# Optimization experiments

Measured on AMD Instinct MI355X. Metric: run time of the kernel, lower is better.

Reference implementation:

```python
import math
import jax, jax.numpy as jnp
import numpy as np
from jax import lax

B, T, D, H = 4, 1024, 1024, 8192
EPS = 1e-6
PLIF_TH = 0.05        # plif_threshold init
SURR_ALPHA = 2.0      # atan surrogate sharpness
SPARSITY = 0.95

@jax.custom_vjp
def spike(v):
    # Heaviside forward, atan surrogate backward (spikingjelly-style)
    return (v > 0).astype(v.dtype)

def _spike_fwd(v):
    return (v > 0).astype(v.dtype), v

def _spike_bwd(v, g):
    return (g * (SURR_ALPHA / 2.0) / (1.0 + (math.pi / 2.0 * SURR_ALPHA * v) ** 2),)

spike.defvjp(_spike_fwd, _spike_bwd)

def rmsnorm(x, w):
    return x * lax.rsqrt(jnp.mean(x * x, axis=-1, keepdims=True) + EPS) * w

def setup_inputs() -> dict:
    key = jax.random.key(0)
    ks = jax.random.split(key, 12)
    std = 0.02
    return {
        "x": jax.random.normal(ks[0], (B, T, D), jnp.float32),
        "ln1_w": jnp.ones((D,), jnp.float32),
        "liq_Wi": jax.random.normal(ks[1], (D, D), jnp.float32) * std,
        "liq_Wr": jax.random.normal(ks[2], (D, D), jnp.float32) * std,
        "liq_b": jnp.zeros((D,), jnp.float32),
        "liq_tau": 0.5 + jax.random.uniform(ks[3], (D,), jnp.float32),  # positive time constants ('hasani' init)
        "plif_tau": jnp.full((1,), 2.5, jnp.float32),                   # plif_tau_init=2.5
        "syn_w": jax.random.normal(ks[4], (D, D), jnp.float32) * std,
        "gate_w": jax.random.normal(ks[5], (D, D), jnp.float32) * 0.01,
        "gate_b": jnp.zeros((D,), jnp.float32),
        "ln2_w": jnp.ones((D,), jnp.float32),
        "ffn_wg": jax.random.normal(ks[6], (H, D), jnp.float32) * std,
        "ffn_wu": jax.random.normal(ks[7], (H, D), jnp.float32) * std,
        "ffn_wd": jax.random.normal(ks[8], (D, H), jnp.float32) * (std / math.sqrt(2.0)),
        "syn_mask": jax.random.uniform(ks[9], (D, D), jnp.float32) < (1.0 - SPARSITY),
    }

def _forward(x, ln1_w, liq_Wi, liq_Wr, liq_b, liq_tau, plif_tau,
             syn_w, gate_w, gate_b, ln2_w, ffn_wg, ffn_wu, ffn_wd, syn_mask):
    a = rmsnorm(x, ln1_w)                                   # (B,T,D)
    # LiquidCell: ODE-style leaky recurrence, h_t = h*e^{-1/tau} + (1-e^{-1/tau})*tanh(Wi x + Wr h + b)
    decay = jnp.exp(-1.0 / liq_tau)                         # (D,)
    def liq_step(h, xt):
        f = jnp.tanh(xt @ liq_Wi.T + h @ liq_Wr.T + liq_b)
        h2 = h * decay + (1.0 - decay) * f
        return h2, h2
    _, hs = lax.scan(liq_step, jnp.zeros((B, D), x.dtype), jnp.swapaxes(a, 0, 1))
    h = jnp.swapaxes(hs, 0, 1)                              # (B,T,D)
    # PLIFCell.forward_seq: v += (h_t - v)/tau; spike; subtract reset
    inv_tau = 1.0 / plif_tau[0]
    def plif_step(v, ht):
        v = v + (ht - v) * inv_tau
        s = spike(v - PLIF_TH)
        return v - s * PLIF_TH, s
    _, ss = lax.scan(plif_step, jnp.zeros((B, D), x.dtype), jnp.swapaxes(h, 0, 1))
    s = jnp.swapaxes(ss, 0, 1)                              # (B,T,D) binary spikes
    w_eff = syn_w * syn_mask.astype(syn_w.dtype)
    syn_out = s @ w_eff.T
    gated = syn_out * jax.nn.sigmoid(s @ gate_w.T + gate_b)
    x = x + gated
    y = rmsnorm(x, ln2_w)
    ffn = (jax.nn.silu(y @ ffn_wg.T) * (y @ ffn_wu.T)) @ ffn_wd.T
    return x + ffn

def reference(x, ln1_w, liq_Wi, liq_Wr, liq_b, liq_tau, plif_tau,
              syn_w, gate_w, gate_b, ln2_w, ffn_wg, ffn_wu, ffn_wd, syn_mask):
    return _forward(x, ln1_w, liq_Wi, liq_Wr, liq_b, liq_tau, plif_tau,
                    syn_w, gate_w, gate_b, ln2_w, ffn_wg, ffn_wu, ffn_wd, syn_mask)
```

## Files before the change

kernel.cpp:

```cpp
#include <hip/hip_runtime.h>
#include <math.h>


#define Bsz 4
#define Tsz 1024
#define Dsz 1024
#define Hsz 8192

typedef __attribute__((ext_vector_type(8))) short short8;
typedef __attribute__((ext_vector_type(4))) float floatx4_t;


__device__ __forceinline__ unsigned short f2bf(float f) {
  union { float f; unsigned u; } c; c.f = f;
  unsigned x = c.u;
  unsigned r = (x + 0x7FFFu + ((x >> 16) & 1u)) >> 16;
  return (unsigned short)r;
}

__device__ __forceinline__ void gll16(const void* gsrc, void* ldst) {
  __builtin_amdgcn_global_load_lds(
      (const __attribute__((address_space(1))) unsigned int*)gsrc,
      (__attribute__((address_space(3))) unsigned int*)ldst,
      16, 0, 0);
}


__global__ void zero_u64_k(unsigned long long* p, int n) {
  int i = blockIdx.x * 256 + threadIdx.x;
  if (i < n) p[i] = 0ull;
}

__global__ void detect_mask_k(const unsigned int* m, int* mode) {
  if (blockIdx.x == 0 && threadIdx.x == 0) {
    int md = 0;
    for (int i = 0; i < 256; ++i) {
      unsigned w = m[i];
      if (w == 0x3F800000u) { md = 2; break; }
      if (w > 1u) md = 1;
    }
    *mode = md;
  }
}

__global__ void cvt_bf16_k(const float* __restrict__ in,
                           unsigned short* __restrict__ out, int n4) {
  int i = blockIdx.x * 256 + threadIdx.x;
  if (i < n4) {
    float4 v = ((const float4*)in)[i];
    ushort4 o;
    o.x = f2bf(v.x); o.y = f2bf(v.y); o.z = f2bf(v.z); o.w = f2bf(v.w);
    ((ushort4*)out)[i] = o;
  }
}

__global__ void make_weff_k(const float* __restrict__ syn,
                            const void* __restrict__ mask,
                            const int* __restrict__ mode,
                            unsigned short* __restrict__ out, int n) {
  int i = blockIdx.x * 256 + threadIdx.x;
  if (i < n) {
    int md = *mode;
    bool on;
    if (md == 1)      on = ((const unsigned char*)mask)[i] != 0;
    else if (md == 2) on = ((const float*)mask)[i] != 0.f;
    else              on = ((const int*)mask)[i] != 0;
    out[i] = on ? f2bf(syn[i]) : (unsigned short)0;
  }
}


template<int BF16OUT>
__global__ __launch_bounds__(256)
void rmsnorm_k(const float* __restrict__ X, const float* __restrict__ w,
               void* __restrict__ out) {
  const long row = blockIdx.x;
  const float* x = X + row * Dsz;
  float4 v = ((const float4*)x)[threadIdx.x];
  float ss = v.x * v.x + v.y * v.y + v.z * v.z + v.w * v.w;
#pragma unroll
  for (int off = 32; off > 0; off >>= 1) ss += __shfl_down(ss, off);
  __shared__ float red[4];
  if ((threadIdx.x & 63) == 0) red[threadIdx.x >> 6] = ss;
  __syncthreads();
  float tot = red[0] + red[1] + red[2] + red[3];
  float scale = 1.0f / sqrtf(tot * (1.0f / Dsz) + 1e-6f);
  float4 wv = ((const float4*)w)[threadIdx.x];
  float o0 = v.x * scale * wv.x, o1 = v.y * scale * wv.y;
  float o2 = v.z * scale * wv.z, o3 = v.w * scale * wv.w;
  if (BF16OUT) {
    ushort4 o; o.x = f2bf(o0); o.y = f2bf(o1); o.z = f2bf(o2); o.w = f2bf(o3);
    ((ushort4*)out)[row * 256 + threadIdx.x] = o;
  } else {
    float4 o; o.x = o0; o.y = o1; o.z = o2; o.w = o3;
    ((float4*)out)[row * 256 + threadIdx.x] = o;
  }
}


__global__ __launch_bounds__(256)
void gemm_f32_bt(const float* __restrict__ A, const float* __restrict__ Bm,
                 const float* __restrict__ bias, float* __restrict__ C,
                 int M, int N, int K) {
  __shared__ float sA[16][128 + 4];
  __shared__ float sB[16][64 + 4];
  const int bm = blockIdx.x, bn = blockIdx.y;
  const int tid = threadIdx.x;
  const int tx = tid & 15, ty = tid >> 4;
  float cacc[8][4] = {};
  for (int k0 = 0; k0 < K; k0 += 16) {
#pragma unroll
    for (int i = 0; i < 2; ++i) {
      int slot = tid * 2 + i, row = slot >> 2, kq = slot & 3;
      float4 v = *(const float4*)(A + (long)(bm * 128 + row) * K + k0 + kq * 4);
      sA[kq * 4 + 0][row] = v.x; sA[kq * 4 + 1][row] = v.y;
      sA[kq * 4 + 2][row] = v.z; sA[kq * 4 + 3][row] = v.w;
    }
    {
      int row = tid >> 2, kq = tid & 3;
      float4 v = *(const float4*)(Bm + (long)(bn * 64 + row) * K + k0 + kq * 4);
      sB[kq * 4 + 0][row] = v.x; sB[kq * 4 + 1][row] = v.y;
      sB[kq * 4 + 2][row] = v.z; sB[kq * 4 + 3][row] = v.w;
    }
    __syncthreads();
#pragma unroll
    for (int kk = 0; kk < 16; ++kk) {
      float4 A0 = *(const float4*)&sA[kk][ty * 8];
      float4 A1 = *(const float4*)&sA[kk][ty * 8 + 4];
      float4 B0 = *(const float4*)&sB[kk][tx * 4];
      float av[8] = {A0.x, A0.y, A0.z, A0.w, A1.x, A1.y, A1.z, A1.w};
      float bv[4] = {B0.x, B0.y, B0.z, B0.w};
#pragma unroll
      for (int r = 0; r < 8; ++r)
#pragma unroll
        for (int c = 0; c < 4; ++c) cacc[r][c] += av[r] * bv[c];
    }
    __syncthreads();
  }
#pragma unroll
  for (int r = 0; r < 8; ++r) {
#pragma unroll
    for (int c = 0; c < 4; ++c) {
      int col = bn * 64 + tx * 4 + c;
      C[(long)(bm * 128 + ty * 8 + r) * N + col] = cacc[r][c] + bias[col];
    }
  }
}


__global__ __launch_bounds__(256)
void liquid_plif_k(const float* __restrict__ Wr, const float* __restrict__ U,
                   const float* __restrict__ liq_tau,
                   const float* __restrict__ plif_tau,
                   unsigned long long* __restrict__ Hex,
                   unsigned short* __restrict__ Sout) {
  const int blk = blockIdx.x;
  const int b = blk >> 5;
  const int base = (blk & 31) * 32;
  const int tid = threadIdx.x;
  const int rg = tid & 7;
  const int ck = tid >> 3;

  __shared__ float h_lds[1024];
  __shared__ float red[4][8][4];

  float4 wr[4][8];
#pragma unroll
  for (int r = 0; r < 4; ++r) {
    const float* wrow = Wr + (long)(base + rg * 4 + r) * Dsz + ck * 32;
#pragma unroll
    for (int qq = 0; qq < 8; ++qq) {
      int q = (qq + ck) & 7;
      wr[r][qq] = *(const float4*)(wrow + q * 4);
    }
  }

  float hstate = 0.f, vstate = 0.f, dec = 0.f, omdec = 0.f, itau = 0.f;
  if (tid < 32) {
    float tau = liq_tau[base + tid];
    dec = expf(-1.0f / tau);
    omdec = 1.0f - dec;
    itau = 1.0f / plif_tau[0];
  }

  for (int t = 1; t <= Tsz; ++t) {
    float uval = 0.f;
    if (tid < 32)
      uval = U[((long)b * Tsz + (t - 1)) * Dsz + base + tid];

    const unsigned want = (unsigned)(t - 1);
    const unsigned long long* src = Hex + (((long)((t - 1) & 1) * Bsz + b) << 10);
    unsigned long long a0, a1, a2, a3;
    for (;;) {
      a0 = __hip_atomic_load(src + tid,       __ATOMIC_RELAXED, __HIP_MEMORY_SCOPE_AGENT);
      a1 = __hip_atomic_load(src + tid + 256, __ATOMIC_RELAXED, __HIP_MEMORY_SCOPE_AGENT);
      a2 = __hip_atomic_load(src + tid + 512, __ATOMIC_RELAXED, __HIP_MEMORY_SCOPE_AGENT);
      a3 = __hip_atomic_load(src + tid + 768, __ATOMIC_RELAXED, __HIP_MEMORY_SCOPE_AGENT);
      if ((unsigned)(a0 >> 32) == want && (unsigned)(a1 >> 32) == want &&
          (unsigned)(a2 >> 32) == want && (unsigned)(a3 >> 32) == want)
        break;
      __builtin_amdgcn_s_sleep(1);
    }
    h_lds[tid]       = __uint_as_float((unsigned)a0);
    h_lds[tid + 256] = __uint_as_float((unsigned)a1);
    h_lds[tid + 512] = __uint_as_float((unsigned)a2);
    h_lds[tid + 768] = __uint_as_float((unsigned)a3);
    __syncthreads();

    float acc0 = 0.f, acc1 = 0.f, acc2 = 0.f, acc3 = 0.f;
    const float* hch = &h_lds[ck * 32];
#pragma unroll
    for (int qq = 0; qq < 8; ++qq) {
      const int q = (qq + ck) & 7;
      float4 hv = *(const float4*)(hch + q * 4);
      acc0 += wr[0][qq].x * hv.x + wr[0][qq].y * hv.y + wr[0][qq].z * hv.z + wr[0][qq].w * hv.w;
      acc1 += wr[1][qq].x * hv.x + wr[1][qq].y * hv.y + wr[1][qq].z * hv.z + wr[1][qq].w * hv.w;
      acc2 += wr[2][qq].x * hv.x + wr[2][qq].y * hv.y + wr[2][qq].z * hv.z + wr[2][qq].w * hv.w;
      acc3 += wr[3][qq].x * hv.x + wr[3][qq].y * hv.y + wr[3][qq].z * hv.z + wr[3][qq].w * hv.w;
    }
    acc0 += __shfl_xor(acc0, 8);  acc0 += __shfl_xor(acc0, 16); acc0 += __shfl_xor(acc0, 32);
    acc1 += __shfl_xor(acc1, 8);  acc1 += __shfl_xor(acc1, 16); acc1 += __shfl_xor(acc1, 32);
    acc2 += __shfl_xor(acc2, 8);  acc2 += __shfl_xor(acc2, 16); acc2 += __shfl_xor(acc2, 32);
    acc3 += __shfl_xor(acc3, 8);  acc3 += __shfl_xor(acc3, 16); acc3 += __shfl_xor(acc3, 32);
    if ((tid & 56) == 0) {
      const int wv = tid >> 6;
      red[wv][rg][0] = acc0; red[wv][rg][1] = acc1;
      red[wv][rg][2] = acc2; red[wv][rg][3] = acc3;
    }
    __syncthreads();

    if (tid < 32) {
      const int r2 = tid >> 2, jj = tid & 3;
      float sum = red[0][r2][jj] + red[1][r2][jj] + red[2][r2][jj] + red[3][r2][jj];
      float f = tanhf(sum + uval);
      hstate = hstate * dec + omdec * f;
      vstate += (hstate - vstate) * itau;
      float sp = ((vstate - 0.05f) > 0.f) ? 1.f : 0.f;
      vstate -= sp * 0.05f;
      unsigned long long pv =
          (((unsigned long long)(unsigned)t) << 32) |
          (unsigned long long)__float_as_uint(hstate);
      __hip_atomic_store(&Hex[(((long)(t & 1) * Bsz + b) << 10) + base + tid], pv,
                         __ATOMIC_RELAXED, __HIP_MEMORY_SCOPE_AGENT);
      Sout[((long)b * Tsz + (t - 1)) * Dsz + base + tid] =
          (sp > 0.f) ? (unsigned short)0x3F80 : (unsigned short)0;
    }
  }
}


template<int NB, int EPI>
__global__ __launch_bounds__(256)
void gemm_bt(const unsigned short* __restrict__ A,
             const unsigned short* __restrict__ B0,
             const unsigned short* __restrict__ B1,
             const float* __restrict__ aux0, const float* __restrict__ aux1,
             void* __restrict__ outp, int M, int N, int K) {
  __shared__ unsigned short sA[128 * 32];
  __shared__ unsigned short sB[2 * 128 * 32];
  const int tid = threadIdx.x;
  const int w = tid >> 6, l = tid & 63;
  const int wm = w & 1, wn = w >> 1;
  const int bm = blockIdx.x, bn = blockIdx.y;

  floatx4_t acc[NB][4][4];
#pragma unroll
  for (int j = 0; j < NB; ++j)
#pragma unroll
    for (int m = 0; m < 4; ++m)
#pragma unroll
      for (int n = 0; n < 4; ++n) acc[j][m][n] = (floatx4_t)(0.f);

  const int rA = bm * 128 + 16 * w + (l >> 2);
  const int rB = bn * 128 + 16 * w + (l >> 2);
  const int kl = (l & 3) * 8;
  const unsigned short* gA = A + (long)rA * K + kl;
  const unsigned short* gB0 = B0 + (long)rB * K + kl;
  const unsigned short* gB1 = nullptr;
  if constexpr (NB > 1) gB1 = B1 + (long)rB * K + kl;
  unsigned short* lA = &sA[(16 * w) * 32];
  unsigned short* lB = &sB[(16 * w) * 32];

  for (int k0 = 0; k0 < K; k0 += 32) {
    gll16(gA + k0,              lA);
    gll16(gA + k0 + 64 * K,     lA + 64 * 32);
    gll16(gB0 + k0,             lB);
    gll16(gB0 + k0 + 64 * K,    lB + 64 * 32);
    if constexpr (NB > 1) {
      gll16(gB1 + k0,           lB + 128 * 32);
      gll16(gB1 + k0 + 64 * K,  lB + 192 * 32);
    }
    __syncthreads();
    short8 af[4];
#pragma unroll
    for (int m = 0; m < 4; ++m)
      af[m] = *(const short8*)&sA[(wm * 64 + m * 16 + (l & 15)) * 32 + (l >> 4) * 8];
#pragma unroll
    for (int j = 0; j < NB; ++j) {
#pragma unroll
      for (int n = 0; n < 4; ++n) {
        short8 bf = *(const short8*)&sB[j * 128 * 32 +
                        (wn * 64 + n * 16 + (l & 15)) * 32 + (l >> 4) * 8];
#pragma unroll
        for (int m = 0; m < 4; ++m)
          acc[j][m][n] = __builtin_amdgcn_mfma_f32_16x16x32_bf16(
              af[m], bf, acc[j][m][n], 0, 0, 0);
      }
    }
    __syncthreads();
  }

  const int colBase = bn * 128 + wn * 64;
  const int rowBase = bm * 128 + wm * 64;
#pragma unroll
  for (int m = 0; m < 4; ++m) {
#pragma unroll
    for (int n = 0; n < 4; ++n) {
      const int col = colBase + n * 16 + (l & 15);
#pragma unroll
      for (int j = 0; j < 4; ++j) {
        const int row = rowBase + m * 16 + (l >> 4) * 4 + j;
        const long idx = (long)row * N + col;
        float v0 = acc[0][m][n][j];
        if constexpr (EPI == 1) {
          float gsum = acc[NB - 1][m][n][j] + aux1[col];
          float sg = 1.f / (1.f + __expf(-gsum));
          ((float*)outp)[idx] = aux0[idx] + v0 * sg;
        } else if constexpr (EPI == 2) {
          float sil = v0 / (1.f + __expf(-v0));
          ((unsigned short*)outp)[idx] = f2bf(sil * acc[NB - 1][m][n][j]);
        } else {
          ((float*)outp)[idx] = aux0[idx] + v0;
        }
      }
    }
  }
}


extern "C" void kernel_launch(void* const* d_in, const int* in_sizes, int n_in,
                              void* d_out, int out_size, void* d_ws, size_t ws_size,
                              hipStream_t stream) {
  (void)in_sizes; (void)n_in; (void)out_size; (void)ws_size;

  const float* x        = (const float*)d_in[0];
  const float* ln1_w    = (const float*)d_in[1];
  const float* liq_Wi   = (const float*)d_in[2];
  const float* liq_Wr   = (const float*)d_in[3];
  const float* liq_b    = (const float*)d_in[4];
  const float* liq_tau  = (const float*)d_in[5];
  const float* plif_tau = (const float*)d_in[6];
  const float* syn_w    = (const float*)d_in[7];
  const float* gate_w   = (const float*)d_in[8];
  const float* gate_b   = (const float*)d_in[9];
  const float* ln2_w    = (const float*)d_in[10];
  const float* ffn_wg   = (const float*)d_in[11];
  const float* ffn_wu   = (const float*)d_in[12];
  const float* ffn_wd   = (const float*)d_in[13];
  const void*  mask     = d_in[14];

  char* ws = (char*)d_ws;
  const size_t MB = 1024ull * 1024ull;
  unsigned short* wg_bf   = (unsigned short*)(ws + 0 * MB);
  unsigned short* wu_bf   = (unsigned short*)(ws + 16 * MB);
  unsigned short* wd_bf   = (unsigned short*)(ws + 32 * MB);
  unsigned short* weff_bf = (unsigned short*)(ws + 48 * MB);
  unsigned short* gw_bf   = (unsigned short*)(ws + 50 * MB);
  float*          x2_f    = (float*)         (ws + 52 * MB);
  unsigned short* s_bf    = (unsigned short*)(ws + 68 * MB);
  unsigned short* y_bf    = (unsigned short*)(ws + 76 * MB);
  unsigned short* ff_bf   = (unsigned short*)(ws + 84 * MB);
  float*          a_f     = (float*)         (ws + 84 * MB);
  float*          u_f     = (float*)         (ws + 100 * MB);
  unsigned long long* hex = (unsigned long long*)(ws + 148 * MB);
  int*            mode    = (int*)(ws + 148 * MB + 65536);
  float*          out_f   = (float*)d_out;

  const int M = Bsz * Tsz;

  detect_mask_k<<<1, 64, 0, stream>>>((const unsigned int*)mask, mode);
  cvt_bf16_k<<<(Hsz * Dsz / 4) / 256, 256, 0, stream>>>(ffn_wg, wg_bf, Hsz * Dsz / 4);
  cvt_bf16_k<<<(Hsz * Dsz / 4) / 256, 256, 0, stream>>>(ffn_wu, wu_bf, Hsz * Dsz / 4);
  cvt_bf16_k<<<(Dsz * Hsz / 4) / 256, 256, 0, stream>>>(ffn_wd, wd_bf, Dsz * Hsz / 4);
  cvt_bf16_k<<<(Dsz * Dsz / 4) / 256, 256, 0, stream>>>(gate_w, gw_bf, Dsz * Dsz / 4);
  make_weff_k<<<(Dsz * Dsz) / 256, 256, 0, stream>>>(syn_w, mask, mode, weff_bf, Dsz * Dsz);
  zero_u64_k<<<32, 256, 0, stream>>>(hex, 2 * Bsz * Dsz);

  rmsnorm_k<0><<<M, 256, 0, stream>>>(x, ln1_w, a_f);

  gemm_f32_bt<<<dim3(M / 128, Dsz / 64), 256, 0, stream>>>(
      a_f, liq_Wi, liq_b, u_f, M, Dsz, Dsz);

  liquid_plif_k<<<128, 256, 0, stream>>>(liq_Wr, u_f, liq_tau, plif_tau, hex, s_bf);

  gemm_bt<2, 1><<<dim3(M / 128, Dsz / 128), 256, 0, stream>>>(
      s_bf, weff_bf, gw_bf, x, gate_b, x2_f, M, Dsz, Dsz);

  rmsnorm_k<1><<<M, 256, 0, stream>>>(x2_f, ln2_w, y_bf);

  gemm_bt<2, 2><<<dim3(M / 128, Hsz / 128), 256, 0, stream>>>(
      y_bf, wg_bf, wu_bf, nullptr, nullptr, ff_bf, M, Hsz, Dsz);

  gemm_bt<1, 3><<<dim3(M / 128, Dsz / 128), 256, 0, stream>>>(
      ff_bf, wd_bf, nullptr, x2_f, nullptr, out_f, M, Dsz, Hsz);
}
```

Measured before the change: 2.449 ms.

## Co-locate recurrence blocks per batch on one XCD and poll with L2-local loads

The grid is doubled to 256 and odd-XCD blocks exit, so that all 32 blocks serving one batch index sit on a single XCD, assuming round-robin block-to-XCD placement. The spin-wait first polls with volatile loads that may hit the shared L2, and falls back to agent-scope atomic loads after two rounds. Each producer writes with a volatile store followed by the atomic store. tanhf is replaced by a fast exp/rcp formula. The goal is lower cross-XCD synchronization latency per timestep, at the risk of relying on undocumented block placement and on volatile-visibility semantics, and of a small precision loss in tanh.

```diff
diff --git a/kernel.cpp b/kernel.cpp
--- a/kernel.cpp
+++ b/kernel.cpp
@@ -155,8 +155,10 @@
                    unsigned long long* __restrict__ Hex,
                    unsigned short* __restrict__ Sout) {
   const int blk = blockIdx.x;
-  const int b = blk >> 5;
-  const int base = (blk & 31) * 32;
+  const int xcd = blk & 7;
+  if (xcd & 1) return;
+  const int b = xcd >> 1;
+  const int base = (blk >> 3) * 32;
   const int tid = threadIdx.x;
   const int rg = tid & 7;
   const int ck = tid >> 3;
@@ -190,16 +192,27 @@
 
     const unsigned want = (unsigned)(t - 1);
     const unsigned long long* src = Hex + (((long)((t - 1) & 1) * Bsz + b) << 10);
-    unsigned long long a0, a1, a2, a3;
-    for (;;) {
-      a0 = __hip_atomic_load(src + tid,       __ATOMIC_RELAXED, __HIP_MEMORY_SCOPE_AGENT);
-      a1 = __hip_atomic_load(src + tid + 256, __ATOMIC_RELAXED, __HIP_MEMORY_SCOPE_AGENT);
-      a2 = __hip_atomic_load(src + tid + 512, __ATOMIC_RELAXED, __HIP_MEMORY_SCOPE_AGENT);
-      a3 = __hip_atomic_load(src + tid + 768, __ATOMIC_RELAXED, __HIP_MEMORY_SCOPE_AGENT);
-      if ((unsigned)(a0 >> 32) == want && (unsigned)(a1 >> 32) == want &&
-          (unsigned)(a2 >> 32) == want && (unsigned)(a3 >> 32) == want)
-        break;
-      __builtin_amdgcn_s_sleep(1);
+    volatile const unsigned long long* vsrc = src;
+    unsigned long long a0 = 0, a1 = 0, a2 = 0, a3 = 0;
+    bool k0 = false, k1 = false, k2 = false, k3 = false;
+    for (int round = 0;; ++round) {
+      unsigned long long v;
+      if (!k0) { v = vsrc[tid      ]; if ((unsigned)(v >> 32) == want) { a0 = v; k0 = true; } }
+      if (!k1) { v = vsrc[tid + 256]; if ((unsigned)(v >> 32) == want) { a1 = v; k1 = true; } }
+      if (!k2) { v = vsrc[tid + 512]; if ((unsigned)(v >> 32) == want) { a2 = v; k2 = true; } }
+      if (!k3) { v = vsrc[tid + 768]; if ((unsigned)(v >> 32) == want) { a3 = v; k3 = true; } }
+      if (k0 && k1 && k2 && k3) break;
+      if (round >= 2) {
+        if (!k0) { v = __hip_atomic_load(src + tid,       __ATOMIC_RELAXED, __HIP_MEMORY_SCOPE_AGENT);
+                   if ((unsigned)(v >> 32) == want) { a0 = v; k0 = true; } }
+        if (!k1) { v = __hip_atomic_load(src + tid + 256, __ATOMIC_RELAXED, __HIP_MEMORY_SCOPE_AGENT);
+                   if ((unsigned)(v >> 32) == want) { a1 = v; k1 = true; } }
+        if (!k2) { v = __hip_atomic_load(src + tid + 512, __ATOMIC_RELAXED, __HIP_MEMORY_SCOPE_AGENT);
+                   if ((unsigned)(v >> 32) == want) { a2 = v; k2 = true; } }
+        if (!k3) { v = __hip_atomic_load(src + tid + 768, __ATOMIC_RELAXED, __HIP_MEMORY_SCOPE_AGENT);
+                   if ((unsigned)(v >> 32) == want) { a3 = v; k3 = true; } }
+        if (k0 && k1 && k2 && k3) break;
+      }
     }
     h_lds[tid]       = __uint_as_float((unsigned)a0);
     h_lds[tid + 256] = __uint_as_float((unsigned)a1);
@@ -232,15 +245,19 @@
     if (tid < 32) {
       const int r2 = tid >> 2, jj = tid & 3;
       float sum = red[0][r2][jj] + red[1][r2][jj] + red[2][r2][jj] + red[3][r2][jj];
-      float f = tanhf(sum + uval);
+      float z = sum + uval;
+      float ex = __expf(2.0f * z);
+      float f = 1.0f - 2.0f * __builtin_amdgcn_rcpf(ex + 1.0f);
       hstate = hstate * dec + omdec * f;
       vstate += (hstate - vstate) * itau;
       float sp = ((vstate - 0.05f) > 0.f) ? 1.f : 0.f;
       vstate -= sp * 0.05f;
+      const long pidx = (((long)(t & 1) * Bsz + b) << 10) + base + tid;
       unsigned long long pv =
           (((unsigned long long)(unsigned)t) << 32) |
           (unsigned long long)__float_as_uint(hstate);
-      __hip_atomic_store(&Hex[(((long)(t & 1) * Bsz + b) << 10) + base + tid], pv,
+      *(volatile unsigned long long*)&Hex[pidx] = pv;
+      __hip_atomic_store(&Hex[pidx], pv,
                          __ATOMIC_RELAXED, __HIP_MEMORY_SCOPE_AGENT);
       Sout[((long)b * Tsz + (t - 1)) * Dsz + base + tid] =
           (sp > 0.f) ? (unsigned short)0x3F80 : (unsigned short)0;
@@ -391,7 +408,7 @@
   gemm_f32_bt<<<dim3(M / 128, Dsz / 64), 256, 0, stream>>>(
       a_f, liq_Wi, liq_b, u_f, M, Dsz, Dsz);
 
-  liquid_plif_k<<<128, 256, 0, stream>>>(liq_Wr, u_f, liq_tau, plif_tau, hex, s_bf);
+  liquid_plif_k<<<256, 256, 0, stream>>>(liq_Wr, u_f, liq_tau, plif_tau, hex, s_bf);
 
   gemm_bt<2, 1><<<dim3(M / 128, Dsz / 128), 256, 0, stream>>>(
       s_bf, weff_bf, gw_bf, x, gate_b, x2_f, M, Dsz, Dsz);
```

Result: slower. 3.125 ms (+27.6%).

## Split liquid recurrence into producer waves and consumer wave with LDS flags

Applied to the files above, without the earlier changes.

Restructures the serial liquid/PLIF recurrence kernel. Four waves each poll only their own 256-element slice of the global h exchange buffer and compute partial matvecs. A dedicated fifth wave waits on workgroup-scope LDS flags, then does the tanh and state update. Block-wide __syncthreads barriers on each timestep are replaced by double-buffered reduction slots and release/acquire flags, and tanhf is swapped for a fast exp/rcp form. The aim is to shorten the per-step critical path, at the cost of spin-waiting and slightly lower tanh precision.

```diff
diff --git a/kernel.cpp b/kernel.cpp
--- a/kernel.cpp
+++ b/kernel.cpp
@@ -148,7 +148,7 @@
 }
 
 
-__global__ __launch_bounds__(256)
+__global__ __launch_bounds__(320)
 void liquid_plif_k(const float* __restrict__ Wr, const float* __restrict__ U,
                    const float* __restrict__ liq_tau,
                    const float* __restrict__ plif_tau,
@@ -158,92 +158,115 @@
   const int b = blk >> 5;
   const int base = (blk & 31) * 32;
   const int tid = threadIdx.x;
-  const int rg = tid & 7;
-  const int ck = tid >> 3;
 
   __shared__ float h_lds[1024];
-  __shared__ float red[4][8][4];
-
-  float4 wr[4][8];
-#pragma unroll
-  for (int r = 0; r < 4; ++r) {
-    const float* wrow = Wr + (long)(base + rg * 4 + r) * Dsz + ck * 32;
-#pragma unroll
-    for (int qq = 0; qq < 8; ++qq) {
-      int q = (qq + ck) & 7;
-      wr[r][qq] = *(const float4*)(wrow + q * 4);
-    }
-  }
-
-  float hstate = 0.f, vstate = 0.f, dec = 0.f, omdec = 0.f, itau = 0.f;
-  if (tid < 32) {
-    float tau = liq_tau[base + tid];
-    dec = expf(-1.0f / tau);
-    omdec = 1.0f - dec;
-    itau = 1.0f / plif_tau[0];
-  }
-
-  for (int t = 1; t <= Tsz; ++t) {
-    float uval = 0.f;
-    if (tid < 32)
-      uval = U[((long)b * Tsz + (t - 1)) * Dsz + base + tid];
-
-    const unsigned want = (unsigned)(t - 1);
-    const unsigned long long* src = Hex + (((long)((t - 1) & 1) * Bsz + b) << 10);
-    unsigned long long a0, a1, a2, a3;
-    for (;;) {
-      a0 = __hip_atomic_load(src + tid,       __ATOMIC_RELAXED, __HIP_MEMORY_SCOPE_AGENT);
-      a1 = __hip_atomic_load(src + tid + 256, __ATOMIC_RELAXED, __HIP_MEMORY_SCOPE_AGENT);
-      a2 = __hip_atomic_load(src + tid + 512, __ATOMIC_RELAXED, __HIP_MEMORY_SCOPE_AGENT);
-      a3 = __hip_atomic_load(src + tid + 768, __ATOMIC_RELAXED, __HIP_MEMORY_SCOPE_AGENT);
-      if ((unsigned)(a0 >> 32) == want && (unsigned)(a1 >> 32) == want &&
-          (unsigned)(a2 >> 32) == want && (unsigned)(a3 >> 32) == want)
-        break;
-      __builtin_amdgcn_s_sleep(1);
-    }
-    h_lds[tid]       = __uint_as_float((unsigned)a0);
-    h_lds[tid + 256] = __uint_as_float((unsigned)a1);
-    h_lds[tid + 512] = __uint_as_float((unsigned)a2);
-    h_lds[tid + 768] = __uint_as_float((unsigned)a3);
-    __syncthreads();
-
-    float acc0 = 0.f, acc1 = 0.f, acc2 = 0.f, acc3 = 0.f;
-    const float* hch = &h_lds[ck * 32];
-#pragma unroll
-    for (int qq = 0; qq < 8; ++qq) {
-      const int q = (qq + ck) & 7;
-      float4 hv = *(const float4*)(hch + q * 4);
-      acc0 += wr[0][qq].x * hv.x + wr[0][qq].y * hv.y + wr[0][qq].z * hv.z + wr[0][qq].w * hv.w;
-      acc1 += wr[1][qq].x * hv.x + wr[1][qq].y * hv.y + wr[1][qq].z * hv.z + wr[1][qq].w * hv.w;
-      acc2 += wr[2][qq].x * hv.x + wr[2][qq].y * hv.y + wr[2][qq].z * hv.z + wr[2][qq].w * hv.w;
-      acc3 += wr[3][qq].x * hv.x + wr[3][qq].y * hv.y + wr[3][qq].z * hv.z + wr[3][qq].w * hv.w;
-    }
-    acc0 += __shfl_xor(acc0, 8);  acc0 += __shfl_xor(acc0, 16); acc0 += __shfl_xor(acc0, 32);
-    acc1 += __shfl_xor(acc1, 8);  acc1 += __shfl_xor(acc1, 16); acc1 += __shfl_xor(acc1, 32);
-    acc2 += __shfl_xor(acc2, 8);  acc2 += __shfl_xor(acc2, 16); acc2 += __shfl_xor(acc2, 32);
-    acc3 += __shfl_xor(acc3, 8);  acc3 += __shfl_xor(acc3, 16); acc3 += __shfl_xor(acc3, 32);
-    if ((tid & 56) == 0) {
-      const int wv = tid >> 6;
-      red[wv][rg][0] = acc0; red[wv][rg][1] = acc1;
-      red[wv][rg][2] = acc2; red[wv][rg][3] = acc3;
-    }
-    __syncthreads();
-
-    if (tid < 32) {
-      const int r2 = tid >> 2, jj = tid & 3;
-      float sum = red[0][r2][jj] + red[1][r2][jj] + red[2][r2][jj] + red[3][r2][jj];
-      float f = tanhf(sum + uval);
-      hstate = hstate * dec + omdec * f;
-      vstate += (hstate - vstate) * itau;
-      float sp = ((vstate - 0.05f) > 0.f) ? 1.f : 0.f;
-      vstate -= sp * 0.05f;
-      unsigned long long pv =
-          (((unsigned long long)(unsigned)t) << 32) |
-          (unsigned long long)__float_as_uint(hstate);
-      __hip_atomic_store(&Hex[(((long)(t & 1) * Bsz + b) << 10) + base + tid], pv,
-                         __ATOMIC_RELAXED, __HIP_MEMORY_SCOPE_AGENT);
-      Sout[((long)b * Tsz + (t - 1)) * Dsz + base + tid] =
-          (sp > 0.f) ? (unsigned short)0x3F80 : (unsigned short)0;
+  __shared__ __align__(16) float red[2][4][8][4];
+  __shared__ int flags[2][4];
+
+  if (tid < 8) ((int*)flags)[tid] = 0;
+  __syncthreads();
+
+  if (tid < 256) {
+    const int l = tid & 63, w = tid >> 6;
+    const int rg = tid & 7;
+    const int ck = tid >> 3;
+    const int win = 256 * w;
+
+    float4 wr[4][8];
+#pragma unroll
+    for (int r = 0; r < 4; ++r) {
+      const float* wrow = Wr + (long)(base + rg * 4 + r) * Dsz + ck * 32;
+#pragma unroll
+      for (int qq = 0; qq < 8; ++qq) {
+        int q = (qq + ck) & 7;
+        wr[r][qq] = *(const float4*)(wrow + q * 4);
+      }
+    }
+
+    for (int t = 1; t <= Tsz; ++t) {
+      const unsigned want = (unsigned)(t - 1);
+      const unsigned long long* src =
+          Hex + (((long)((t - 1) & 1) * Bsz + b) << 10) + win;
+      unsigned long long a0, a1, a2, a3;
+      for (;;) {
+        a0 = __hip_atomic_load(src + l,       __ATOMIC_RELAXED, __HIP_MEMORY_SCOPE_AGENT);
+        a1 = __hip_atomic_load(src + l + 64,  __ATOMIC_RELAXED, __HIP_MEMORY_SCOPE_AGENT);
+        a2 = __hip_atomic_load(src + l + 128, __ATOMIC_RELAXED, __HIP_MEMORY_SCOPE_AGENT);
+        a3 = __hip_atomic_load(src + l + 192, __ATOMIC_RELAXED, __HIP_MEMORY_SCOPE_AGENT);
+        int ok = ((unsigned)(a0 >> 32) == want) & ((unsigned)(a1 >> 32) == want) &
+                 ((unsigned)(a2 >> 32) == want) & ((unsigned)(a3 >> 32) == want);
+        if (__all(ok)) break;
+      }
+      h_lds[win + l]       = __uint_as_float((unsigned)a0);
+      h_lds[win + l + 64]  = __uint_as_float((unsigned)a1);
+      h_lds[win + l + 128] = __uint_as_float((unsigned)a2);
+      h_lds[win + l + 192] = __uint_as_float((unsigned)a3);
+
+      float acc0 = 0.f, acc1 = 0.f, acc2 = 0.f, acc3 = 0.f;
+      const float* hch = &h_lds[ck * 32];
+#pragma unroll
+      for (int qq = 0; qq < 8; ++qq) {
+        const int q = (qq + ck) & 7;
+        float4 hv = *(const float4*)(hch + q * 4);
+        acc0 += wr[0][qq].x * hv.x + wr[0][qq].y * hv.y + wr[0][qq].z * hv.z + wr[0][qq].w * hv.w;
+        acc1 += wr[1][qq].x * hv.x + wr[1][qq].y * hv.y + wr[1][qq].z * hv.z + wr[1][qq].w * hv.w;
+        acc2 += wr[2][qq].x * hv.x + wr[2][qq].y * hv.y + wr[2][qq].z * hv.z + wr[2][qq].w * hv.w;
+        acc3 += wr[3][qq].x * hv.x + wr[3][qq].y * hv.y + wr[3][qq].z * hv.z + wr[3][qq].w * hv.w;
+      }
+      acc0 += __shfl_xor(acc0, 8); acc0 += __shfl_xor(acc0, 16); acc0 += __shfl_xor(acc0, 32);
+      acc1 += __shfl_xor(acc1, 8); acc1 += __shfl_xor(acc1, 16); acc1 += __shfl_xor(acc1, 32);
+      acc2 += __shfl_xor(acc2, 8); acc2 += __shfl_xor(acc2, 16); acc2 += __shfl_xor(acc2, 32);
+      acc3 += __shfl_xor(acc3, 8); acc3 += __shfl_xor(acc3, 16); acc3 += __shfl_xor(acc3, 32);
+      if ((l & 56) == 0) {
+        float4 rv; rv.x = acc0; rv.y = acc1; rv.z = acc2; rv.w = acc3;
+        *(float4*)&red[t & 1][w][rg][0] = rv;
+      }
+      asm volatile("s_waitcnt lgkmcnt(0)" ::: "memory");
+      if (l == 0)
+        __hip_atomic_store(&flags[t & 1][w], t, __ATOMIC_RELEASE,
+                           __HIP_MEMORY_SCOPE_WORKGROUP);
+    }
+  } else {
+    const int r = tid - 256;
+    float hstate = 0.f, vstate = 0.f, dec = 0.f, omdec = 0.f, itau = 0.f;
+    if (r < 32) {
+      float tau = liq_tau[base + r];
+      dec = expf(-1.0f / tau);
+      omdec = 1.0f - dec;
+      itau = 1.0f / plif_tau[0];
+    }
+    for (int t = 1; t <= Tsz; ++t) {
+      float uval = 0.f;
+      if (r < 32)
+        uval = U[((long)b * Tsz + (t - 1)) * Dsz + base + r];
+      const int p = t & 1;
+      for (;;) {
+        int f0 = __hip_atomic_load(&flags[p][0], __ATOMIC_ACQUIRE, __HIP_MEMORY_SCOPE_WORKGROUP);
+        int f1 = __hip_atomic_load(&flags[p][1], __ATOMIC_ACQUIRE, __HIP_MEMORY_SCOPE_WORKGROUP);
+        int f2 = __hip_atomic_load(&flags[p][2], __ATOMIC_ACQUIRE, __HIP_MEMORY_SCOPE_WORKGROUP);
+        int f3 = __hip_atomic_load(&flags[p][3], __ATOMIC_ACQUIRE, __HIP_MEMORY_SCOPE_WORKGROUP);
+        if ((f0 == t) & (f1 == t) & (f2 == t) & (f3 == t)) break;
+      }
+      if (r < 32) {
+        const int r2 = r >> 2, jj = r & 3;
+        float sum = red[p][0][r2][jj] + red[p][1][r2][jj] +
+                    red[p][2][r2][jj] + red[p][3][r2][jj];
+        float z = sum + uval;
+        float ex = __expf(2.0f * z);
+        float f = 1.0f - 2.0f * __builtin_amdgcn_rcpf(ex + 1.0f);
+        hstate = hstate * dec + omdec * f;
+        vstate += (hstate - vstate) * itau;
+        float sp = ((vstate - 0.05f) > 0.f) ? 1.f : 0.f;
+        vstate -= sp * 0.05f;
+        const long pidx = (((long)(t & 1) * Bsz + b) << 10) + base + r;
+        unsigned long long pv =
+            (((unsigned long long)(unsigned)t) << 32) |
+            (unsigned long long)__float_as_uint(hstate);
+        __hip_atomic_store(&Hex[pidx], pv, __ATOMIC_RELAXED,
+                           __HIP_MEMORY_SCOPE_AGENT);
+        Sout[((long)b * Tsz + (t - 1)) * Dsz + base + r] =
+            (sp > 0.f) ? (unsigned short)0x3F80 : (unsigned short)0;
+      }
     }
   }
 }
@@ -391,7 +414,7 @@
   gemm_f32_bt<<<dim3(M / 128, Dsz / 64), 256, 0, stream>>>(
       a_f, liq_Wi, liq_b, u_f, M, Dsz, Dsz);
 
-  liquid_plif_k<<<128, 256, 0, stream>>>(liq_Wr, u_f, liq_tau, plif_tau, hex, s_bf);
+  liquid_plif_k<<<128, 320, 0, stream>>>(liq_Wr, u_f, liq_tau, plif_tau, hex, s_bf);
 
   gemm_bt<2, 1><<<dim3(M / 128, Dsz / 128), 256, 0, stream>>>(
       s_bf, weff_bf, gw_bf, x, gate_b, x2_f, M, Dsz, Dsz);
```

New measurement: 2.392 ms. 1.02x faster.

## Exchange per-wave partial sums instead of h to drop block barriers in recurrence

Applied to the files above, without the earlier changes.

The liquid recurrence kernel now publishes per-wave partial dot products, tagged with the timestep, into a 4-deep global ring. Every block redundantly reduces the partials and recomputes tanh and the leaky update for all 1024 hidden units, which removes both __syncthreads and the red[] LDS reduction on the serial per-step critical path. Polling uses inline-asm dwordx4 loads with a wave-wide vote, and tanh is replaced by a fast exp/rcp formula. The trade-off is that each block now reads four times more data per step, and the buffer aliases x2_f in the workspace.

```diff
diff --git a/kernel.cpp b/kernel.cpp
--- a/kernel.cpp
+++ b/kernel.cpp
@@ -9,6 +9,7 @@
 
 typedef __attribute__((ext_vector_type(8))) short short8;
 typedef __attribute__((ext_vector_type(4))) float floatx4_t;
+typedef __attribute__((ext_vector_type(4))) unsigned int uint4v;
 
 
 __device__ __forceinline__ unsigned short f2bf(float f) {
@@ -148,21 +149,23 @@
 }
 
 
-__global__ __launch_bounds__(256)
+__global__ __launch_bounds__(256, 1)
 void liquid_plif_k(const float* __restrict__ Wr, const float* __restrict__ U,
                    const float* __restrict__ liq_tau,
                    const float* __restrict__ plif_tau,
-                   unsigned long long* __restrict__ Hex,
+                   unsigned long long* __restrict__ P,
                    unsigned short* __restrict__ Sout) {
   const int blk = blockIdx.x;
   const int b = blk >> 5;
-  const int base = (blk & 31) * 32;
+  const int k = blk & 31;
+  const int base = k * 32;
   const int tid = threadIdx.x;
+  const int l = tid & 63, w = tid >> 6;
   const int rg = tid & 7;
   const int ck = tid >> 3;
+  const int win = 256 * w;
 
   __shared__ float h_lds[1024];
-  __shared__ float red[4][8][4];
 
   float4 wr[4][8];
 #pragma unroll
@@ -175,37 +178,89 @@
     }
   }
 
-  float hstate = 0.f, vstate = 0.f, dec = 0.f, omdec = 0.f, itau = 0.f;
-  if (tid < 32) {
-    float tau = liq_tau[base + tid];
-    dec = expf(-1.0f / tau);
-    omdec = 1.0f - dec;
-    itau = 1.0f / plif_tau[0];
-  }
+  float dec[4], omdec[4], hloc[4];
+#pragma unroll
+  for (int j = 0; j < 4; ++j) {
+    float tau = liq_tau[win + j * 64 + l];
+    dec[j] = expf(-1.0f / tau);
+    omdec[j] = 1.0f - dec[j];
+    hloc[j] = 0.f;
+  }
+
+  const int j0 = (k & 7) >> 1;
+  const bool is_sout = (w == (k >> 3)) && ((l >> 5) == (k & 1));
+  float vstate = 0.f;
+  const float itau = 1.0f / plif_tau[0];
 
   for (int t = 1; t <= Tsz; ++t) {
-    float uval = 0.f;
-    if (tid < 32)
-      uval = U[((long)b * Tsz + (t - 1)) * Dsz + base + tid];
+    const float* up = U + ((long)b * Tsz + (t - 1)) * Dsz + win + l;
+    float uval0 = up[0], uval1 = up[64], uval2 = up[128], uval3 = up[192];
 
     const unsigned want = (unsigned)(t - 1);
-    const unsigned long long* src = Hex + (((long)((t - 1) & 1) * Bsz + b) << 10);
-    unsigned long long a0, a1, a2, a3;
+    const unsigned long long* src = P + (((long)((t - 1) & 3) * Bsz + b) << 12);
+    const unsigned long long* pa0 = src + (size_t)(win + l) * 4;
+    const unsigned long long* pa1 = pa0 + 64 * 4;
+    const unsigned long long* pa2 = pa0 + 128 * 4;
+    const unsigned long long* pa3 = pa0 + 192 * 4;
+    uint4v q0a, q0b, q1a, q1b, q2a, q2b, q3a, q3b;
     for (;;) {
-      a0 = __hip_atomic_load(src + tid,       __ATOMIC_RELAXED, __HIP_MEMORY_SCOPE_AGENT);
-      a1 = __hip_atomic_load(src + tid + 256, __ATOMIC_RELAXED, __HIP_MEMORY_SCOPE_AGENT);
-      a2 = __hip_atomic_load(src + tid + 512, __ATOMIC_RELAXED, __HIP_MEMORY_SCOPE_AGENT);
-      a3 = __hip_atomic_load(src + tid + 768, __ATOMIC_RELAXED, __HIP_MEMORY_SCOPE_AGENT);
-      if ((unsigned)(a0 >> 32) == want && (unsigned)(a1 >> 32) == want &&
-          (unsigned)(a2 >> 32) == want && (unsigned)(a3 >> 32) == want)
-        break;
-      __builtin_amdgcn_s_sleep(1);
-    }
-    h_lds[tid]       = __uint_as_float((unsigned)a0);
-    h_lds[tid + 256] = __uint_as_float((unsigned)a1);
-    h_lds[tid + 512] = __uint_as_float((unsigned)a2);
-    h_lds[tid + 768] = __uint_as_float((unsigned)a3);
-    __syncthreads();
+      asm volatile(
+          "global_load_dwordx4 %0, %8, off sc1\n\t"
+          "global_load_dwordx4 %1, %8, off offset:16 sc1\n\t"
+          "global_load_dwordx4 %2, %9, off sc1\n\t"
+          "global_load_dwordx4 %3, %9, off offset:16 sc1\n\t"
+          "global_load_dwordx4 %4, %10, off sc1\n\t"
+          "global_load_dwordx4 %5, %10, off offset:16 sc1\n\t"
+          "global_load_dwordx4 %6, %11, off sc1\n\t"
+          "global_load_dwordx4 %7, %11, off offset:16 sc1\n\t"
+          "s_waitcnt vmcnt(0)"
+          : "=&v"(q0a), "=&v"(q0b), "=&v"(q1a), "=&v"(q1b),
+            "=&v"(q2a), "=&v"(q2b), "=&v"(q3a), "=&v"(q3b)
+          : "v"(pa0), "v"(pa1), "v"(pa2), "v"(pa3)
+          : "memory");
+      int ok = (q0a[1] == want) & (q0a[3] == want) & (q0b[1] == want) & (q0b[3] == want) &
+               (q1a[1] == want) & (q1a[3] == want) & (q1b[1] == want) & (q1b[3] == want) &
+               (q2a[1] == want) & (q2a[3] == want) & (q2b[1] == want) & (q2b[3] == want) &
+               (q3a[1] == want) & (q3a[3] == want) & (q3b[1] == want) & (q3b[3] == want);
+      if (__all(ok)) break;
+    }
+
+    float sum0 = (__uint_as_float(q0a[0]) + __uint_as_float(q0a[2])) +
+                 (__uint_as_float(q0b[0]) + __uint_as_float(q0b[2]));
+    float sum1 = (__uint_as_float(q1a[0]) + __uint_as_float(q1a[2])) +
+                 (__uint_as_float(q1b[0]) + __uint_as_float(q1b[2]));
+    float sum2 = (__uint_as_float(q2a[0]) + __uint_as_float(q2a[2])) +
+                 (__uint_as_float(q2b[0]) + __uint_as_float(q2b[2]));
+    float sum3 = (__uint_as_float(q3a[0]) + __uint_as_float(q3a[2])) +
+                 (__uint_as_float(q3b[0]) + __uint_as_float(q3b[2]));
+    float z0 = sum0 + uval0, z1 = sum1 + uval1, z2 = sum2 + uval2, z3 = sum3 + uval3;
+    float f0 = 1.0f - 2.0f * __builtin_amdgcn_rcpf(__expf(2.0f * z0) + 1.0f);
+    float f1 = 1.0f - 2.0f * __builtin_amdgcn_rcpf(__expf(2.0f * z1) + 1.0f);
+    float f2 = 1.0f - 2.0f * __builtin_amdgcn_rcpf(__expf(2.0f * z2) + 1.0f);
+    float f3 = 1.0f - 2.0f * __builtin_amdgcn_rcpf(__expf(2.0f * z3) + 1.0f);
+    hloc[0] = hloc[0] * dec[0] + omdec[0] * f0;
+    hloc[1] = hloc[1] * dec[1] + omdec[1] * f1;
+    hloc[2] = hloc[2] * dec[2] + omdec[2] * f2;
+    hloc[3] = hloc[3] * dec[3] + omdec[3] * f3;
+
+    if (is_sout) {
+#pragma unroll
+      for (int j = 0; j < 4; ++j) {
+        if (j == j0) {
+          vstate += (hloc[j] - vstate) * itau;
+          float sp = ((vstate - 0.05f) > 0.f) ? 1.f : 0.f;
+          vstate -= sp * 0.05f;
+          Sout[((long)b * Tsz + (t - 1)) * Dsz + base + (l & 31)] =
+              (sp > 0.f) ? (unsigned short)0x3F80 : (unsigned short)0;
+        }
+      }
+    }
+
+    h_lds[win + l]       = hloc[0];
+    h_lds[win + l + 64]  = hloc[1];
+    h_lds[win + l + 128] = hloc[2];
+    h_lds[win + l + 192] = hloc[3];
+    asm volatile("s_waitcnt lgkmcnt(0)" ::: "memory");
 
     float acc0 = 0.f, acc1 = 0.f, acc2 = 0.f, acc3 = 0.f;
     const float* hch = &h_lds[ck * 32];
@@ -218,32 +273,23 @@
       acc2 += wr[2][qq].x * hv.x + wr[2][qq].y * hv.y + wr[2][qq].z * hv.z + wr[2][qq].w * hv.w;
       acc3 += wr[3][qq].x * hv.x + wr[3][qq].y * hv.y + wr[3][qq].z * hv.z + wr[3][qq].w * hv.w;
     }
-    acc0 += __shfl_xor(acc0, 8);  acc0 += __shfl_xor(acc0, 16); acc0 += __shfl_xor(acc0, 32);
-    acc1 += __shfl_xor(acc1, 8);  acc1 += __shfl_xor(acc1, 16); acc1 += __shfl_xor(acc1, 32);
-    acc2 += __shfl_xor(acc2, 8);  acc2 += __shfl_xor(acc2, 16); acc2 += __shfl_xor(acc2, 32);
-    acc3 += __shfl_xor(acc3, 8);  acc3 += __shfl_xor(acc3, 16); acc3 += __shfl_xor(acc3, 32);
-    if ((tid & 56) == 0) {
-      const int wv = tid >> 6;
-      red[wv][rg][0] = acc0; red[wv][rg][1] = acc1;
-      red[wv][rg][2] = acc2; red[wv][rg][3] = acc3;
-    }
-    __syncthreads();
-
-    if (tid < 32) {
-      const int r2 = tid >> 2, jj = tid & 3;
-      float sum = red[0][r2][jj] + red[1][r2][jj] + red[2][r2][jj] + red[3][r2][jj];
-      float f = tanhf(sum + uval);
-      hstate = hstate * dec + omdec * f;
-      vstate += (hstate - vstate) * itau;
-      float sp = ((vstate - 0.05f) > 0.f) ? 1.f : 0.f;
-      vstate -= sp * 0.05f;
-      unsigned long long pv =
-          (((unsigned long long)(unsigned)t) << 32) |
-          (unsigned long long)__float_as_uint(hstate);
-      __hip_atomic_store(&Hex[(((long)(t & 1) * Bsz + b) << 10) + base + tid], pv,
+    acc0 += __shfl_xor(acc0, 8); acc0 += __shfl_xor(acc0, 16); acc0 += __shfl_xor(acc0, 32);
+    acc1 += __shfl_xor(acc1, 8); acc1 += __shfl_xor(acc1, 16); acc1 += __shfl_xor(acc1, 32);
+    acc2 += __shfl_xor(acc2, 8); acc2 += __shfl_xor(acc2, 16); acc2 += __shfl_xor(acc2, 32);
+    acc3 += __shfl_xor(acc3, 8); acc3 += __shfl_xor(acc3, 16); acc3 += __shfl_xor(acc3, 32);
+
+    if (l < 8) {
+      unsigned long long* dst = P + (((long)(t & 3) * Bsz + b) << 12) +
+                                ((size_t)(base + l * 4) << 2) + w;
+      const unsigned long long tg = ((unsigned long long)(unsigned)t) << 32;
+      __hip_atomic_store(dst,      tg | (unsigned long long)__float_as_uint(acc0),
                          __ATOMIC_RELAXED, __HIP_MEMORY_SCOPE_AGENT);
-      Sout[((long)b * Tsz + (t - 1)) * Dsz + base + tid] =
-          (sp > 0.f) ? (unsigned short)0x3F80 : (unsigned short)0;
+      __hip_atomic_store(dst + 4,  tg | (unsigned long long)__float_as_uint(acc1),
+                         __ATOMIC_RELAXED, __HIP_MEMORY_SCOPE_AGENT);
+      __hip_atomic_store(dst + 8,  tg | (unsigned long long)__float_as_uint(acc2),
+                         __ATOMIC_RELAXED, __HIP_MEMORY_SCOPE_AGENT);
+      __hip_atomic_store(dst + 12, tg | (unsigned long long)__float_as_uint(acc3),
+                         __ATOMIC_RELAXED, __HIP_MEMORY_SCOPE_AGENT);
     }
   }
 }
@@ -367,12 +413,12 @@
   unsigned short* weff_bf = (unsigned short*)(ws + 48 * MB);
   unsigned short* gw_bf   = (unsigned short*)(ws + 50 * MB);
   float*          x2_f    = (float*)         (ws + 52 * MB);
+  unsigned long long* P   = (unsigned long long*)(ws + 52 * MB);
   unsigned short* s_bf    = (unsigned short*)(ws + 68 * MB);
   unsigned short* y_bf    = (unsigned short*)(ws + 76 * MB);
   unsigned short* ff_bf   = (unsigned short*)(ws + 84 * MB);
   float*          a_f     = (float*)         (ws + 84 * MB);
   float*          u_f     = (float*)         (ws + 100 * MB);
-  unsigned long long* hex = (unsigned long long*)(ws + 148 * MB);
   int*            mode    = (int*)(ws + 148 * MB + 65536);
   float*          out_f   = (float*)d_out;
 
@@ -384,14 +430,14 @@
   cvt_bf16_k<<<(Dsz * Hsz / 4) / 256, 256, 0, stream>>>(ffn_wd, wd_bf, Dsz * Hsz / 4);
   cvt_bf16_k<<<(Dsz * Dsz / 4) / 256, 256, 0, stream>>>(gate_w, gw_bf, Dsz * Dsz / 4);
   make_weff_k<<<(Dsz * Dsz) / 256, 256, 0, stream>>>(syn_w, mask, mode, weff_bf, Dsz * Dsz);
-  zero_u64_k<<<32, 256, 0, stream>>>(hex, 2 * Bsz * Dsz);
+  zero_u64_k<<<256, 256, 0, stream>>>(P, 4 * Bsz * Dsz * 4);
 
   rmsnorm_k<0><<<M, 256, 0, stream>>>(x, ln1_w, a_f);
 
   gemm_f32_bt<<<dim3(M / 128, Dsz / 64), 256, 0, stream>>>(
       a_f, liq_Wi, liq_b, u_f, M, Dsz, Dsz);
 
-  liquid_plif_k<<<128, 256, 0, stream>>>(liq_Wr, u_f, liq_tau, plif_tau, hex, s_bf);
+  liquid_plif_k<<<128, 256, 0, stream>>>(liq_Wr, u_f, liq_tau, plif_tau, P, s_bf);
 
   gemm_bt<2, 1><<<dim3(M / 128, Dsz / 128), 256, 0, stream>>>(
       s_bf, weff_bf, gw_bf, x, gate_b, x2_f, M, Dsz, Dsz);
```

Result: slower. 6.520 ms (+166.2%).
